# Performance work log

Hardware: AMD Instinct MI355X
Metric: run time of the kernel (lower is better)

## Reference

```python
import jax, jax.numpy as jnp
import numpy as np

B, S, D, V = 4, 512, 512, 32000
GAMMA = 0.5
EPS = 1e-12  # torch F.normalize clamp_min eps


def _l2norm(x, axis):
    n = jnp.sqrt(jnp.sum(x * x, axis=axis, keepdims=True))
    return x / jnp.maximum(n, EPS)


def setup_inputs() -> dict:
    key = jax.random.key(0)
    k1, k2, k3 = jax.random.split(key, 3)
    preds = jax.random.normal(k1, (B, D, S), dtype=jnp.float32)
    emb_weight = jax.random.normal(k2, (V, D), dtype=jnp.float32)
    target = jax.random.randint(k3, (B, S), 0, V, dtype=jnp.int64)
    return {"preds": preds, "emb_weight": emb_weight, "target": target, "pad_id": 0}


def reference(preds, emb_weight, target, pad_id):
    # preds: [B, D, S] -> [B, S, D], L2-normalized over D
    out_norm = _l2norm(jnp.transpose(preds, (0, 2, 1)), axis=2)
    voc_norm = _l2norm(emb_weight, axis=1)          # [V, D]
    tgt_emb = emb_weight[target]                     # [B, S, D] (raw lookup, not normalized)
    mask = target != pad_id                          # [B, S]

    cos_out_voc = jnp.einsum('bsd,vd->bsv', out_norm, voc_norm)  # [B, S, V]
    tgt_voc = jnp.einsum('bsd,vd->bsv', tgt_emb, voc_norm)       # [B, S, V]

    jmax = jnp.argmax(cos_out_voc - tgt_voc, axis=2)             # [B, S]
    cos_target = jnp.take_along_axis(cos_out_voc, target[..., None], axis=2)[..., 0]
    max_cos_voc = jnp.take_along_axis(cos_out_voc, jmax[..., None], axis=2)[..., 0]

    diff = jnp.maximum(GAMMA + max_cos_voc - cos_target, 0.0)    # [B, S]
    denom = jnp.sum(mask).astype(diff.dtype)
    return jnp.sum(jnp.where(mask, diff, 0.0)) / denom
```

## Files before the change

### kernel.cpp

```cpp
#include <hip/hip_runtime.h>
#include <math.h>


#define Bb 4
#define Ss 512
#define Dd 512
#define Vv 32000
#define ROWS (Bb * Ss)
#define NTILE_M (ROWS / 128)
#define NTILE_N (Vv / 128)

typedef __attribute__((ext_vector_type(8))) short bf16x8;
typedef __attribute__((ext_vector_type(4))) float f32x4;

__device__ __forceinline__ float waveReduceSum(float x) {
#pragma unroll
  for (int m = 32; m >= 1; m >>= 1) x += __shfl_xor(x, m, 64);
  return x;
}

__device__ __forceinline__ unsigned short f2bf(float f) {
  unsigned u = __float_as_uint(f);
  unsigned r = (u + 0x7FFFu + ((u >> 16) & 1u)) >> 16;
  return (unsigned short)r;
}

__device__ __forceinline__ unsigned long long packSC(float s, int c) {
  unsigned b = __float_as_uint(s);
  unsigned key = b ^ ((b & 0x80000000u) ? 0xFFFFFFFFu : 0x80000000u);
  return ((unsigned long long)key << 32) | (unsigned)(~c);
}

__device__ __forceinline__ void async_ld16(const void* g, void* l) {
  __builtin_amdgcn_global_load_lds((const __attribute__((address_space(1))) void*)g,
                                   (__attribute__((address_space(3))) void*)l, 16, 0, 0);
}

__global__ __launch_bounds__(256) void prep_rows(
    const float* __restrict__ preds, const float* __restrict__ emb,
    const int* __restrict__ target,
    float* __restrict__ o_rows, short* __restrict__ u_bf,
    float* __restrict__ cos_tgt) {
  int row0 = blockIdx.x * 4;
  int b = row0 >> 9, s0 = row0 & (Ss - 1);
  int tid = threadIdx.x;
  int wave = tid >> 6, lane = tid & 63;
  const float* p = preds + (size_t)b * Dd * Ss;
  float4 x0 = *(const float4*)(p + (size_t)tid * Ss + s0);
  float4 x1 = *(const float4*)(p + (size_t)(tid + 256) * Ss + s0);
  float a0[4] = {x0.x, x0.y, x0.z, x0.w};
  float a1[4] = {x1.x, x1.y, x1.z, x1.w};
  __shared__ float rA[4][4], rB[4][4], rC[4][4];
  float sq[4];
#pragma unroll
  for (int j = 0; j < 4; ++j) sq[j] = waveReduceSum(a0[j] * a0[j] + a1[j] * a1[j]);
  if (lane == 0)
#pragma unroll
    for (int j = 0; j < 4; ++j) rA[wave][j] = sq[j];
  __syncthreads();
  float o0[4], o1[4];
#pragma unroll
  for (int j = 0; j < 4; ++j) {
    float inv = 1.0f / fmaxf(sqrtf(rA[0][j] + rA[1][j] + rA[2][j] + rA[3][j]), 1e-12f);
    o0[j] = a0[j] * inv;
    o1[j] = a1[j] * inv;
    o_rows[(size_t)(row0 + j) * Dd + tid] = o0[j];
    o_rows[(size_t)(row0 + j) * Dd + tid + 256] = o1[j];
  }
  float ss2[4], dt[4];
#pragma unroll
  for (int j = 0; j < 4; ++j) {
    int t = target[row0 + j];
    const float* et = emb + (size_t)t * Dd;
    float e0 = et[tid], e1 = et[tid + 256];
    u_bf[(size_t)(row0 + j) * Dd + tid] = (short)f2bf(o0[j] - e0);
    u_bf[(size_t)(row0 + j) * Dd + tid + 256] = (short)f2bf(o1[j] - e1);
    ss2[j] = waveReduceSum(e0 * e0 + e1 * e1);
    dt[j] = waveReduceSum(o0[j] * e0 + o1[j] * e1);
  }
  if (lane == 0)
#pragma unroll
    for (int j = 0; j < 4; ++j) { rB[wave][j] = ss2[j]; rC[wave][j] = dt[j]; }
  __syncthreads();
  if (tid < 4) {
    int j = tid;
    float n2 = rB[0][j] + rB[1][j] + rB[2][j] + rB[3][j];
    float dd = rC[0][j] + rC[1][j] + rC[2][j] + rC[3][j];
    cos_tgt[row0 + j] = dd * (1.0f / fmaxf(sqrtf(n2), 1e-12f));
  }
}

__global__ __launch_bounds__(256) void voc_prep(const float* __restrict__ emb,
                                                short* __restrict__ ebf,
                                                float* __restrict__ inv_norm) {
  int v = blockIdx.x * 4 + (threadIdx.x >> 6);
  int lane = threadIdx.x & 63;
  const float* e = emb + (size_t)v * Dd;
  float4 x0 = *(const float4*)(e + lane * 8);
  float4 x1 = *(const float4*)(e + lane * 8 + 4);
  float ss = x0.x * x0.x + x0.y * x0.y + x0.z * x0.z + x0.w * x0.w +
             x1.x * x1.x + x1.y * x1.y + x1.z * x1.z + x1.w * x1.w;
  ss = waveReduceSum(ss);
  float inv = 1.0f / fmaxf(sqrtf(ss), 1e-12f);
  bf16x8 o;
  o[0] = (short)f2bf(x0.x * inv); o[1] = (short)f2bf(x0.y * inv);
  o[2] = (short)f2bf(x0.z * inv); o[3] = (short)f2bf(x0.w * inv);
  o[4] = (short)f2bf(x1.x * inv); o[5] = (short)f2bf(x1.y * inv);
  o[6] = (short)f2bf(x1.z * inv); o[7] = (short)f2bf(x1.w * inv);
  *(bf16x8*)(ebf + (size_t)v * Dd + lane * 8) = o;
  if (lane == 0) inv_norm[v] = inv;
}

__global__ __launch_bounds__(256) void gemm_argmax(
    const short* __restrict__ u_bf, const short* __restrict__ ebf,
    unsigned long long* __restrict__ part) {
  __shared__ short sA[128 * 64];
  __shared__ short sB[128 * 64];
  int bid = blockIdx.x;
  int g = (bid & 7) * 500 + (bid >> 3);
  int tm = g & 15, tn = g >> 4;
  int tid = threadIdx.x;
  int w = tid >> 6, lane = tid & 63;
  int wm = w >> 1, wn = w & 1;

  int srow = w * 8 + (lane >> 3);
  int schunk = (lane & 7) ^ ((lane >> 3) & 7);
  const short* gA = u_bf + (size_t)(tm * 128 + srow) * Dd + schunk * 8;
  const short* gB = ebf + (size_t)(tn * 128 + srow) * Dd + schunk * 8;

  int fr = lane & 15;
  int q = lane >> 4;
  int ck0 = ((q) ^ (fr & 7)) * 8;
  int ck1 = ((4 + q) ^ (fr & 7)) * 8;

  f32x4 acc[4][4];
  f32x4 z = {0.f, 0.f, 0.f, 0.f};
#pragma unroll
  for (int mi = 0; mi < 4; ++mi)
#pragma unroll
    for (int ni = 0; ni < 4; ++ni) acc[mi][ni] = z;

  for (int kk = 0; kk < Dd / 64; ++kk) {
    __syncthreads();
    {
      const short* ga = gA + kk * 64;
      const short* gb = gB + kk * 64;
#pragma unroll
      for (int i = 0; i < 4; ++i) {
        async_ld16(ga + (size_t)(i * 32) * Dd, &sA[(w * 8 + i * 32) * 64]);
        async_ld16(gb + (size_t)(i * 32) * Dd, &sB[(w * 8 + i * 32) * 64]);
      }
    }
    __syncthreads();
    bf16x8 af0[4], af1[4], bg0[4], bg1[4];
#pragma unroll
    for (int mi = 0; mi < 4; ++mi) {
      int r = (wm * 64 + mi * 16 + fr) * 64;
      af0[mi] = *(const bf16x8*)(sA + r + ck0);
      af1[mi] = *(const bf16x8*)(sA + r + ck1);
    }
#pragma unroll
    for (int ni = 0; ni < 4; ++ni) {
      int r = (wn * 64 + ni * 16 + fr) * 64;
      bg0[ni] = *(const bf16x8*)(sB + r + ck0);
      bg1[ni] = *(const bf16x8*)(sB + r + ck1);
    }
#pragma unroll
    for (int mi = 0; mi < 4; ++mi)
#pragma unroll
      for (int ni = 0; ni < 4; ++ni)
        acc[mi][ni] = __builtin_amdgcn_mfma_f32_16x16x32_bf16(af0[mi], bg0[ni], acc[mi][ni], 0, 0, 0);
#pragma unroll
    for (int mi = 0; mi < 4; ++mi)
#pragma unroll
      for (int ni = 0; ni < 4; ++ni)
        acc[mi][ni] = __builtin_amdgcn_mfma_f32_16x16x32_bf16(af1[mi], bg1[ni], acc[mi][ni], 0, 0, 0);
  }

  float bs[4][4];
  int bc[4][4];
  int col0 = tn * 128 + wn * 64 + (lane & 15);
#pragma unroll
  for (int mi = 0; mi < 4; ++mi) {
#pragma unroll
    for (int j = 0; j < 4; ++j) { bs[mi][j] = acc[mi][0][j]; bc[mi][j] = col0; }
#pragma unroll
    for (int ni = 1; ni < 4; ++ni) {
      int c = col0 + ni * 16;
#pragma unroll
      for (int j = 0; j < 4; ++j) {
        float v = acc[mi][ni][j];
        if (v > bs[mi][j]) { bs[mi][j] = v; bc[mi][j] = c; }
      }
    }
  }
#pragma unroll
  for (int m = 1; m < 16; m <<= 1) {
#pragma unroll
    for (int mi = 0; mi < 4; ++mi)
#pragma unroll
      for (int j = 0; j < 4; ++j) {
        float os = __shfl_xor(bs[mi][j], m, 64);
        int oc = __shfl_xor(bc[mi][j], m, 64);
        if (os > bs[mi][j] || (os == bs[mi][j] && oc < bc[mi][j])) {
          bs[mi][j] = os;
          bc[mi][j] = oc;
        }
      }
  }
  __syncthreads();
  float* sEs = (float*)sA;
  int* sEc = (int*)sA + 256;
  if ((lane & 15) == 0) {
    int qq = lane >> 4;
#pragma unroll
    for (int mi = 0; mi < 4; ++mi)
#pragma unroll
      for (int j = 0; j < 4; ++j) {
        int rloc = wm * 64 + mi * 16 + qq * 4 + j;
        sEs[wn * 128 + rloc] = bs[mi][j];
        sEc[wn * 128 + rloc] = bc[mi][j];
      }
  }
  __syncthreads();
  if (tid < 128) {
    float s0 = sEs[tid], s1 = sEs[128 + tid];
    int c0 = sEc[tid], c1 = sEc[128 + tid];
    if (s1 > s0 || (s1 == s0 && c1 < c0)) { s0 = s1; c0 = c1; }
    part[(size_t)tn * ROWS + tm * 128 + tid] = packSC(s0, c0);
  }
}

__global__ __launch_bounds__(256) void row_final(
    const float* __restrict__ o_rows, const float* __restrict__ emb,
    const float* __restrict__ inv_norm, const float* __restrict__ cos_tgt,
    const int* __restrict__ target, const int* __restrict__ pad_id,
    const unsigned long long* __restrict__ part, float* __restrict__ diffs) {
  int wave = threadIdx.x >> 6, lane = threadIdx.x & 63;
  int row = blockIdx.x * 4 + wave;
  unsigned long long best = 0ull;
  for (int t = lane; t < NTILE_N; t += 64) {
    unsigned long long p = part[(size_t)t * ROWS + row];
    if (p > best) best = p;
  }
#pragma unroll
  for (int m = 1; m < 64; m <<= 1) {
    unsigned long long o = __shfl_xor(best, m, 64);
    if (o > best) best = o;
  }
  int bi = (int)(~(unsigned)(best & 0xFFFFFFFFull));
  const float* o = o_rows + (size_t)row * Dd;
  const float* e = emb + (size_t)bi * Dd;
  float d = 0.f;
#pragma unroll
  for (int i = 0; i < Dd / 64; ++i) d += o[lane + 64 * i] * e[lane + 64 * i];
  d = waveReduceSum(d);
  if (lane == 0) {
    float cmax = d * inv_norm[bi];
    int t = target[row];
    float df = fmaxf(0.5f + cmax - cos_tgt[row], 0.0f);
    diffs[row] = (t != pad_id[0]) ? df : 0.0f;
  }
}

__global__ __launch_bounds__(256) void reduce_final(
    const float* __restrict__ diffs, const int* __restrict__ target,
    const int* __restrict__ pad_id, float* __restrict__ out) {
  int tid = threadIdx.x;
  int pid = pad_id[0];
  float s = 0.f, c = 0.f;
  for (int i = tid; i < ROWS; i += 256) {
    s += diffs[i];
    c += (target[i] != pid) ? 1.0f : 0.0f;
  }
  s = waveReduceSum(s);
  c = waveReduceSum(c);
  __shared__ float rs[4], rc[4];
  int wave = tid >> 6, lane = tid & 63;
  if (lane == 0) { rs[wave] = s; rc[wave] = c; }
  __syncthreads();
  if (tid == 0) out[0] = (rs[0] + rs[1] + rs[2] + rs[3]) / (rc[0] + rc[1] + rc[2] + rc[3]);
}

extern "C" void kernel_launch(void* const* d_in, const int* in_sizes, int n_in,
                              void* d_out, int out_size, void* d_ws, size_t ws_size,
                              hipStream_t stream) {
  const float* preds = (const float*)d_in[0];
  const float* emb = (const float*)d_in[1];
  const int* target = (const int*)d_in[2];
  const int* pad_id = (const int*)d_in[3];
  char* ws = (char*)d_ws;
  float* o_rows = (float*)ws;
  short* u_bf = (short*)(ws + 4194304);
  short* ebf = (short*)(ws + 6291456);
  float* inv_norm = (float*)(ws + 39059456);
  float* cos_tgt = (float*)(ws + 39187456);
  unsigned long long* part = (unsigned long long*)(ws + 39195648);
  float* diffs = (float*)(ws + 43291648);

  prep_rows<<<ROWS / 4, 256, 0, stream>>>(preds, emb, target, o_rows, u_bf, cos_tgt);
  voc_prep<<<Vv / 4, 256, 0, stream>>>(emb, ebf, inv_norm);
  gemm_argmax<<<NTILE_M * NTILE_N, 256, 0, stream>>>(u_bf, ebf, part);
  row_final<<<ROWS / 4, 256, 0, stream>>>(o_rows, emb, inv_norm, cos_tgt, target,
                                          pad_id, part, diffs);
  reduce_final<<<1, 256, 0, stream>>>(diffs, target, pad_id, (float*)d_out);
}
```

Measured before the change: 220.0 us.

## Fuse prep kernels, atomic argmax merge, and fold final reduction into row kernel

Merges the row-prep and vocab-prep kernels into one launch, with block 0 zeroing the result and accumulator buffers. The GEMM epilogue now merges its per-tile packed score/index with a 64-bit atomicMax into a per-row slot, instead of writing a partial array that row_final had to scan. The final row kernel accumulates the masked loss sum and count with atomics, and the last block writes the quotient, which removes the single-block reduce launch. This cuts two launches and the partial-buffer traffic, at the cost of heavy atomic contention on 2048 addresses and an atomic accumulation order that is not deterministic.

```diff
diff --git a/kernel.cpp b/kernel.cpp
--- a/kernel.cpp
+++ b/kernel.cpp
@@ -9,6 +9,7 @@
 #define ROWS (Bb * Ss)
 #define NTILE_M (ROWS / 128)
 #define NTILE_N (Vv / 128)
+#define VOC_BLOCKS (Vv / 4)
 
 typedef __attribute__((ext_vector_type(8))) short bf16x8;
 typedef __attribute__((ext_vector_type(4))) float f32x4;
@@ -36,84 +37,85 @@
                                    (__attribute__((address_space(3))) void*)l, 16, 0, 0);
 }
 
-__global__ __launch_bounds__(256) void prep_rows(
+__global__ __launch_bounds__(256) void prep_all(
     const float* __restrict__ preds, const float* __restrict__ emb,
     const int* __restrict__ target,
     float* __restrict__ o_rows, short* __restrict__ u_bf,
-    float* __restrict__ cos_tgt) {
-  int row0 = blockIdx.x * 4;
-  int b = row0 >> 9, s0 = row0 & (Ss - 1);
+    float* __restrict__ cos_tgt, short* __restrict__ ebf,
+    float* __restrict__ inv_norm, unsigned long long* __restrict__ zero_region) {
   int tid = threadIdx.x;
   int wave = tid >> 6, lane = tid & 63;
-  const float* p = preds + (size_t)b * Dd * Ss;
-  float4 x0 = *(const float4*)(p + (size_t)tid * Ss + s0);
-  float4 x1 = *(const float4*)(p + (size_t)(tid + 256) * Ss + s0);
-  float a0[4] = {x0.x, x0.y, x0.z, x0.w};
-  float a1[4] = {x1.x, x1.y, x1.z, x1.w};
-  __shared__ float rA[4][4], rB[4][4], rC[4][4];
-  float sq[4];
-#pragma unroll
-  for (int j = 0; j < 4; ++j) sq[j] = waveReduceSum(a0[j] * a0[j] + a1[j] * a1[j]);
-  if (lane == 0)
-#pragma unroll
-    for (int j = 0; j < 4; ++j) rA[wave][j] = sq[j];
-  __syncthreads();
-  float o0[4], o1[4];
-#pragma unroll
-  for (int j = 0; j < 4; ++j) {
-    float inv = 1.0f / fmaxf(sqrtf(rA[0][j] + rA[1][j] + rA[2][j] + rA[3][j]), 1e-12f);
-    o0[j] = a0[j] * inv;
-    o1[j] = a1[j] * inv;
-    o_rows[(size_t)(row0 + j) * Dd + tid] = o0[j];
-    o_rows[(size_t)(row0 + j) * Dd + tid + 256] = o1[j];
-  }
-  float ss2[4], dt[4];
-#pragma unroll
-  for (int j = 0; j < 4; ++j) {
-    int t = target[row0 + j];
-    const float* et = emb + (size_t)t * Dd;
-    float e0 = et[tid], e1 = et[tid + 256];
-    u_bf[(size_t)(row0 + j) * Dd + tid] = (short)f2bf(o0[j] - e0);
-    u_bf[(size_t)(row0 + j) * Dd + tid + 256] = (short)f2bf(o1[j] - e1);
-    ss2[j] = waveReduceSum(e0 * e0 + e1 * e1);
-    dt[j] = waveReduceSum(o0[j] * e0 + o1[j] * e1);
-  }
-  if (lane == 0)
-#pragma unroll
-    for (int j = 0; j < 4; ++j) { rB[wave][j] = ss2[j]; rC[wave][j] = dt[j]; }
-  __syncthreads();
-  if (tid < 4) {
-    int j = tid;
-    float n2 = rB[0][j] + rB[1][j] + rB[2][j] + rB[3][j];
-    float dd = rC[0][j] + rC[1][j] + rC[2][j] + rC[3][j];
-    cos_tgt[row0 + j] = dd * (1.0f / fmaxf(sqrtf(n2), 1e-12f));
-  }
-}
-
-__global__ __launch_bounds__(256) void voc_prep(const float* __restrict__ emb,
-                                                short* __restrict__ ebf,
-                                                float* __restrict__ inv_norm) {
-  int v = blockIdx.x * 4 + (threadIdx.x >> 6);
-  int lane = threadIdx.x & 63;
-  const float* e = emb + (size_t)v * Dd;
-  float4 x0 = *(const float4*)(e + lane * 8);
-  float4 x1 = *(const float4*)(e + lane * 8 + 4);
-  float ss = x0.x * x0.x + x0.y * x0.y + x0.z * x0.z + x0.w * x0.w +
-             x1.x * x1.x + x1.y * x1.y + x1.z * x1.z + x1.w * x1.w;
-  ss = waveReduceSum(ss);
-  float inv = 1.0f / fmaxf(sqrtf(ss), 1e-12f);
-  bf16x8 o;
-  o[0] = (short)f2bf(x0.x * inv); o[1] = (short)f2bf(x0.y * inv);
-  o[2] = (short)f2bf(x0.z * inv); o[3] = (short)f2bf(x0.w * inv);
-  o[4] = (short)f2bf(x1.x * inv); o[5] = (short)f2bf(x1.y * inv);
-  o[6] = (short)f2bf(x1.z * inv); o[7] = (short)f2bf(x1.w * inv);
-  *(bf16x8*)(ebf + (size_t)v * Dd + lane * 8) = o;
-  if (lane == 0) inv_norm[v] = inv;
+  if (blockIdx.x < VOC_BLOCKS) {
+    if (blockIdx.x == 0) {
+      for (int i = tid; i < ROWS + 2; i += 256) zero_region[i] = 0ull;
+    }
+    int v = blockIdx.x * 4 + wave;
+    const float* e = emb + (size_t)v * Dd;
+    float4 x0 = *(const float4*)(e + lane * 8);
+    float4 x1 = *(const float4*)(e + lane * 8 + 4);
+    float ss = x0.x * x0.x + x0.y * x0.y + x0.z * x0.z + x0.w * x0.w +
+               x1.x * x1.x + x1.y * x1.y + x1.z * x1.z + x1.w * x1.w;
+    ss = waveReduceSum(ss);
+    float inv = 1.0f / fmaxf(sqrtf(ss), 1e-12f);
+    bf16x8 o;
+    o[0] = (short)f2bf(x0.x * inv); o[1] = (short)f2bf(x0.y * inv);
+    o[2] = (short)f2bf(x0.z * inv); o[3] = (short)f2bf(x0.w * inv);
+    o[4] = (short)f2bf(x1.x * inv); o[5] = (short)f2bf(x1.y * inv);
+    o[6] = (short)f2bf(x1.z * inv); o[7] = (short)f2bf(x1.w * inv);
+    *(bf16x8*)(ebf + (size_t)v * Dd + lane * 8) = o;
+    if (lane == 0) inv_norm[v] = inv;
+  } else {
+    int row0 = (blockIdx.x - VOC_BLOCKS) * 4;
+    int b = row0 >> 9, s0 = row0 & (Ss - 1);
+    const float* p = preds + (size_t)b * Dd * Ss;
+    float4 x0 = *(const float4*)(p + (size_t)tid * Ss + s0);
+    float4 x1 = *(const float4*)(p + (size_t)(tid + 256) * Ss + s0);
+    float a0[4] = {x0.x, x0.y, x0.z, x0.w};
+    float a1[4] = {x1.x, x1.y, x1.z, x1.w};
+    __shared__ float rA[4][4], rB[4][4], rC[4][4];
+    float sq[4];
+#pragma unroll
+    for (int j = 0; j < 4; ++j) sq[j] = waveReduceSum(a0[j] * a0[j] + a1[j] * a1[j]);
+    if (lane == 0)
+#pragma unroll
+      for (int j = 0; j < 4; ++j) rA[wave][j] = sq[j];
+    __syncthreads();
+    float o0[4], o1[4];
+#pragma unroll
+    for (int j = 0; j < 4; ++j) {
+      float inv = 1.0f / fmaxf(sqrtf(rA[0][j] + rA[1][j] + rA[2][j] + rA[3][j]), 1e-12f);
+      o0[j] = a0[j] * inv;
+      o1[j] = a1[j] * inv;
+      o_rows[(size_t)(row0 + j) * Dd + tid] = o0[j];
+      o_rows[(size_t)(row0 + j) * Dd + tid + 256] = o1[j];
+    }
+    float ss2[4], dt[4];
+#pragma unroll
+    for (int j = 0; j < 4; ++j) {
+      int t = target[row0 + j];
+      const float* et = emb + (size_t)t * Dd;
+      float e0 = et[tid], e1 = et[tid + 256];
+      u_bf[(size_t)(row0 + j) * Dd + tid] = (short)f2bf(o0[j] - e0);
+      u_bf[(size_t)(row0 + j) * Dd + tid + 256] = (short)f2bf(o1[j] - e1);
+      ss2[j] = waveReduceSum(e0 * e0 + e1 * e1);
+      dt[j] = waveReduceSum(o0[j] * e0 + o1[j] * e1);
+    }
+    if (lane == 0)
+#pragma unroll
+      for (int j = 0; j < 4; ++j) { rB[wave][j] = ss2[j]; rC[wave][j] = dt[j]; }
+    __syncthreads();
+    if (tid < 4) {
+      int j = tid;
+      float n2 = rB[0][j] + rB[1][j] + rB[2][j] + rB[3][j];
+      float dd = rC[0][j] + rC[1][j] + rC[2][j] + rC[3][j];
+      cos_tgt[row0 + j] = dd * (1.0f / fmaxf(sqrtf(n2), 1e-12f));
+    }
+  }
 }
 
 __global__ __launch_bounds__(256) void gemm_argmax(
     const short* __restrict__ u_bf, const short* __restrict__ ebf,
-    unsigned long long* __restrict__ part) {
+    unsigned long long* __restrict__ best) {
   __shared__ short sA[128 * 64];
   __shared__ short sB[128 * 64];
   int bid = blockIdx.x;
@@ -227,59 +229,46 @@
     float s0 = sEs[tid], s1 = sEs[128 + tid];
     int c0 = sEc[tid], c1 = sEc[128 + tid];
     if (s1 > s0 || (s1 == s0 && c1 < c0)) { s0 = s1; c0 = c1; }
-    part[(size_t)tn * ROWS + tm * 128 + tid] = packSC(s0, c0);
-  }
-}
-
-__global__ __launch_bounds__(256) void row_final(
+    atomicMax(&best[tm * 128 + tid], packSC(s0, c0));
+  }
+}
+
+__global__ __launch_bounds__(256) void row_final_reduce(
     const float* __restrict__ o_rows, const float* __restrict__ emb,
     const float* __restrict__ inv_norm, const float* __restrict__ cos_tgt,
     const int* __restrict__ target, const int* __restrict__ pad_id,
-    const unsigned long long* __restrict__ part, float* __restrict__ diffs) {
+    const unsigned long long* __restrict__ best, float* __restrict__ accum,
+    float* __restrict__ out) {
   int wave = threadIdx.x >> 6, lane = threadIdx.x & 63;
   int row = blockIdx.x * 4 + wave;
-  unsigned long long best = 0ull;
-  for (int t = lane; t < NTILE_N; t += 64) {
-    unsigned long long p = part[(size_t)t * ROWS + row];
-    if (p > best) best = p;
-  }
-#pragma unroll
-  for (int m = 1; m < 64; m <<= 1) {
-    unsigned long long o = __shfl_xor(best, m, 64);
-    if (o > best) best = o;
-  }
-  int bi = (int)(~(unsigned)(best & 0xFFFFFFFFull));
+  int bi = (int)(~(unsigned)(best[row] & 0xFFFFFFFFull));
   const float* o = o_rows + (size_t)row * Dd;
   const float* e = emb + (size_t)bi * Dd;
   float d = 0.f;
 #pragma unroll
   for (int i = 0; i < Dd / 64; ++i) d += o[lane + 64 * i] * e[lane + 64 * i];
   d = waveReduceSum(d);
+  __shared__ float sdf[4], scn[4];
   if (lane == 0) {
     float cmax = d * inv_norm[bi];
     int t = target[row];
     float df = fmaxf(0.5f + cmax - cos_tgt[row], 0.0f);
-    diffs[row] = (t != pad_id[0]) ? df : 0.0f;
-  }
-}
-
-__global__ __launch_bounds__(256) void reduce_final(
-    const float* __restrict__ diffs, const int* __restrict__ target,
-    const int* __restrict__ pad_id, float* __restrict__ out) {
-  int tid = threadIdx.x;
-  int pid = pad_id[0];
-  float s = 0.f, c = 0.f;
-  for (int i = tid; i < ROWS; i += 256) {
-    s += diffs[i];
-    c += (target[i] != pid) ? 1.0f : 0.0f;
-  }
-  s = waveReduceSum(s);
-  c = waveReduceSum(c);
-  __shared__ float rs[4], rc[4];
-  int wave = tid >> 6, lane = tid & 63;
-  if (lane == 0) { rs[wave] = s; rc[wave] = c; }
+    bool ok = (t != pad_id[0]);
+    sdf[wave] = ok ? df : 0.0f;
+    scn[wave] = ok ? 1.0f : 0.0f;
+  }
   __syncthreads();
-  if (tid == 0) out[0] = (rs[0] + rs[1] + rs[2] + rs[3]) / (rc[0] + rc[1] + rc[2] + rc[3]);
+  if (threadIdx.x == 0) {
+    atomicAdd(&accum[0], sdf[0] + sdf[1] + sdf[2] + sdf[3]);
+    atomicAdd(&accum[1], scn[0] + scn[1] + scn[2] + scn[3]);
+    __threadfence();
+    unsigned t = (unsigned)atomicAdd(&accum[2], 1.0f);
+    if (t == (unsigned)(ROWS / 4 - 1)) {
+      __threadfence();
+      volatile float* va = accum;
+      out[0] = va[0] / va[1];
+    }
+  }
 }
 
 extern "C" void kernel_launch(void* const* d_in, const int* in_sizes, int n_in,
@@ -295,13 +284,14 @@
   short* ebf = (short*)(ws + 6291456);
   float* inv_norm = (float*)(ws + 39059456);
   float* cos_tgt = (float*)(ws + 39187456);
-  unsigned long long* part = (unsigned long long*)(ws + 39195648);
-  float* diffs = (float*)(ws + 43291648);
-
-  prep_rows<<<ROWS / 4, 256, 0, stream>>>(preds, emb, target, o_rows, u_bf, cos_tgt);
-  voc_prep<<<Vv / 4, 256, 0, stream>>>(emb, ebf, inv_norm);
-  gemm_argmax<<<NTILE_M * NTILE_N, 256, 0, stream>>>(u_bf, ebf, part);
-  row_final<<<ROWS / 4, 256, 0, stream>>>(o_rows, emb, inv_norm, cos_tgt, target,
-                                          pad_id, part, diffs);
-  reduce_final<<<1, 256, 0, stream>>>(diffs, target, pad_id, (float*)d_out);
-}
+  unsigned long long* best = (unsigned long long*)(ws + 39195648);
+  float* accum = (float*)(ws + 39212032);
+
+  prep_all<<<VOC_BLOCKS + ROWS / 4, 256, 0, stream>>>(preds, emb, target, o_rows,
+                                                      u_bf, cos_tgt, ebf, inv_norm,
+                                                      best);
+  gemm_argmax<<<NTILE_M * NTILE_N, 256, 0, stream>>>(u_bf, ebf, best);
+  row_final_reduce<<<ROWS / 4, 256, 0, stream>>>(o_rows, emb, inv_norm, cos_tgt,
+                                                 target, pad_id, best, accum,
+                                                 (float*)d_out);
+}
```

Measured after the change: 235.5 us. 1.07x slower.
